# Performance work log

Measured on AMD Instinct MI355X. Metric: run time of the kernel, lower is better.

The kernel has to match this reference:

```python
import jax, jax.numpy as jnp
import numpy as np

N = 131072; B = 4; PER = N // B
M = 32768; MPER = M // B; K = 16; E = M * K
NF = 16; C = 32
BNC = float(1.0 / np.sqrt(1.0 + 1e-5))  # BatchNorm1d in eval mode, default running stats (mean=0,var=1,affine=identity)
_kd = np.array([[1.,1.,1.],[-1.,1.,1.],[1.,-1.,1.],[1.,1.,-1.],[-1.,-1.,1.],[-1.,1.,-1.],[1.,-1.,-1.],[-1.,-1.,-1.]], np.float32) / np.float32(np.sqrt(3.0))
KDIRS = jnp.asarray(_kd)  # [8,3] LightKernel directions


def _ln(x, g, b):
    m = x.mean(-1, keepdims=True)
    v = ((x - m) ** 2).mean(-1, keepdims=True)
    return (x - m) / jnp.sqrt(v + 1e-5) * g + b


def _mlp2(x, w1, b1, w2, b2):
    # Seq(Lin, BN, SiLU) x2 ; BN in eval mode == multiply by BNC
    h = jax.nn.silu(BNC * (x @ w1 + b1))
    return jax.nn.silu(BNC * (h @ w2 + b2))


def setup_inputs():
    rng = np.random.default_rng(0)
    f32 = np.float32
    w = lambda fi, fo: jnp.asarray((rng.standard_normal((fi, fo)) * 0.05).astype(f32))
    dg = lambda n: jnp.asarray((rng.standard_normal(n) * 0.05).astype(f32))
    z = lambda n: jnp.zeros((n,), jnp.float32)
    o = lambda n: jnp.ones((n,), jnp.float32)
    pos = jnp.asarray((rng.standard_normal((N, 3)) * 5.0).astype(f32))
    reflectance = jnp.asarray(rng.random(N).astype(f32))
    batch = jnp.asarray(np.repeat(np.arange(B), PER).astype(np.int64))
    sf = jnp.full((B,), 10.0, jnp.float32)
    # voxel-sampled centers: MPER per cloud, within each cloud's index range
    idx = np.concatenate([b * PER + rng.choice(PER, MPER, replace=False) for b in range(B)])
    tb = np.repeat(np.arange(B), MPER)
    # radius-graph edges: K in-batch source neighbors per sampled target
    col = (rng.integers(0, PER, size=(M, K)) + tb[:, None] * PER).reshape(-1)
    row = np.repeat(np.arange(M), K)
    inp = dict(pos=pos, reflectance=reflectance, sf=sf,
               batch=batch, idx=jnp.asarray(idx.astype(np.int64)),
               col=jnp.asarray(col.astype(np.int64)), row=jnp.asarray(row.astype(np.int64)))
    inp.update(stem_ln_g=o(97), stem_ln_b=z(97), stem_w1=w(97, 64), stem_b1=z(64),
               stem_w2=w(64, C), stem_b2=z(C),
               lk_w=w(8, 3), lk_b=z(3), lk_ln_g=o(3), lk_ln_b=z(3),
               loc_w1=w(C + 7, 64), loc_b1=z(64), loc_w2=w(64, 4 * C), loc_b2=z(4 * C),
               exp_w=w(128, 512), exp_b=z(512),
               dw1_w=dg(512), dw1_b=z(512), pw1_w=w(512, 512), pw1_b=z(512),
               dw2_w=dg(512), dw2_b=z(512), pw2_w=w(512, 512), pw2_b=z(512),
               proj_w=w(512, 128), proj_b=z(128))
    return inp


def _forward(pos, reflectance, sf, batch, idx, col, row,
             stem_ln_g, stem_ln_b, stem_w1, stem_b1, stem_w2, stem_b2,
             lk_w, lk_b, lk_ln_g, lk_ln_b,
             loc_w1, loc_b1, loc_w2, loc_b2,
             exp_w, exp_b, dw1_w, dw1_b, pw1_w, pw1_b,
             dw2_w, dw2_b, pw2_w, pw2_b, proj_w, proj_b):
    # --- StemModule: positional encoding + LayerNorm(97) + MLP[97,64,32] ---
    npos = pos / sf[batch][:, None]
    cnt = jax.ops.segment_sum(jnp.ones((N,), jnp.float32), batch, num_segments=B)
    centers = jax.ops.segment_sum(npos, batch, num_segments=B) / jnp.maximum(cnt, 1.0)[:, None]
    npos = npos - centers[batch]
    freqs = 1.0 / (10000.0 ** (2.0 * jnp.arange(NF, dtype=jnp.float32) / NF))
    pe = npos[:, :, None] * freqs                                   # [N,3,NF]
    pe = jnp.concatenate([jnp.sin(pe), jnp.cos(pe)], axis=-1).reshape(N, -1)  # [N,96]
    xin = _ln(jnp.concatenate([pe, reflectance[:, None]], axis=1), stem_ln_g, stem_ln_b)
    x = _mlp2(xin, stem_w1, stem_b1, stem_w2, stem_b2)              # [N,C]
    # --- SAModule: PointNetConv on precomputed radius graph ---
    pos4 = jnp.concatenate([pos, reflectance[:, None]], axis=1)     # [N,4]
    rel = pos4[col] - pos4[idx][row]                                # [E,4] pos_j - pos_i
    rel3 = rel[:, :3]
    dirs = rel3 / (jnp.linalg.norm(rel3, axis=1, keepdims=True) + 1e-8)
    kr = dirs @ KDIRS.T                                             # [E,8] kernel responses
    ecnt = jax.ops.segment_sum(jnp.ones((E,), jnp.float32), row, num_segments=M)
    nb = jax.ops.segment_sum(kr, row, num_segments=M) / jnp.maximum(ecnt, 1.0)[:, None]  # scatter_mean
    sfeat = _ln(nb @ lk_w + lk_b, lk_ln_g, lk_ln_b)                 # [M,3]
    msg = jnp.concatenate([x[col], rel, sfeat[row]], axis=1)        # [E,C+7]
    h = _mlp2(msg, loc_w1, loc_b1, loc_w2, loc_b2)                  # [E,4C] local_nn
    agg = jax.ops.segment_max(h, row, num_segments=M)               # max aggregation [M,4C]
    # --- InvertedResidualBlock (all kernel-size-1 convs => linear / per-channel) ---
    r = agg
    o = jax.nn.silu(BNC * (agg @ exp_w + exp_b))        # expand 128->512
    o = jax.nn.silu(BNC * (o * dw1_w + dw1_b))          # depthwise conv k=1
    o = jax.nn.silu(BNC * (o @ pw1_w + pw1_b))          # pointwise conv
    o = jax.nn.silu(BNC * o)                            # BN+SiLU between DWSep blocks
    o = jax.nn.silu(BNC * (o * dw2_w + dw2_b))
    o = jax.nn.silu(BNC * (o @ pw2_w + pw2_b))
    o = BNC * o                                         # trailing BN (no act)
    o = BNC * (o @ proj_w + proj_b)                     # project 512->128 + BN
    return jax.nn.silu(o + r)                           # [M,4C]


def reference(pos, reflectance, sf, batch, idx, col, row,
              stem_ln_g, stem_ln_b, stem_w1, stem_b1, stem_w2, stem_b2,
              lk_w, lk_b, lk_ln_g, lk_ln_b,
              loc_w1, loc_b1, loc_w2, loc_b2,
              exp_w, exp_b, dw1_w, dw1_b, pw1_w, pw1_b,
              dw2_w, dw2_b, pw2_w, pw2_b, proj_w, proj_b):
    return _forward(pos, reflectance, sf, batch, idx, col, row,
                    stem_ln_g, stem_ln_b, stem_w1, stem_b1, stem_w2, stem_b2,
                    lk_w, lk_b, lk_ln_g, lk_ln_b,
                    loc_w1, loc_b1, loc_w2, loc_b2,
                    exp_w, exp_b, dw1_w, dw1_b, pw1_w, pw1_b,
                    dw2_w, dw2_b, pw2_w, pw2_b, proj_w, proj_b)
```

## Files before the change

kernel.cpp:

```cpp
#include <hip/hip_runtime.h>

typedef unsigned short u16;
typedef unsigned int   u32;
typedef __attribute__((ext_vector_type(8))) u16  u16x8;
typedef __attribute__((ext_vector_type(4))) float f32x4;

#define N_PTS   131072
#define M_PTS   32768
#define BNCF    0.9999950000374997f

__device__ __forceinline__ float b2f(u16 u) {
    u32 x = ((u32)u) << 16;
    float f;
    __builtin_memcpy(&f, &x, 4);
    return f;
}
__device__ __forceinline__ u16 f2b(float f) {
    u32 x;
    __builtin_memcpy(&x, &f, 4);
    u32 r = x + 0x7fffu + ((x >> 16) & 1u);
    return (u16)(r >> 16);
}
__device__ __forceinline__ u16 f2b_hw(float f) {
    u32 r;
    asm("v_cvt_pk_bf16_f32 %0, %1, %1" : "=v"(r) : "v"(f));
    return (u16)r;
}
__device__ __forceinline__ float silu_f(float x) {
    return x * __builtin_amdgcn_rcpf(1.0f + __expf(-x));
}

__device__ __forceinline__ f32x4 mfma_bf16(u16x8 a, u16x8 b, f32x4 c) {
    asm volatile("v_mfma_f32_16x16x32_bf16 %0, %1, %2, %0"
                 : "+v"(c) : "v"(a), "v"(b));
    return c;
}
__device__ __forceinline__ void mai_guard() {
    asm volatile("s_nop 7\n\ts_nop 7\n\ts_nop 3");
}

__device__ __forceinline__ void cp_glds16(const u16* g, u16* l) {
    typedef const __attribute__((address_space(1))) u32* gp1_t;
    typedef __attribute__((address_space(3))) u32* lp3_t;
    __builtin_amdgcn_global_load_lds((gp1_t)(unsigned long long)g,
                                     (lp3_t)(unsigned long long)l, 16, 0, 0);
}

__global__ __launch_bounds__(256) void k_prep(const float* __restrict__ expw, u16* __restrict__ expwt,
                                              const float* __restrict__ pw1w, u16* __restrict__ pw1t,
                                              const float* __restrict__ pw2w, u16* __restrict__ pw2t,
                                              const float* __restrict__ prjw, u16* __restrict__ prjt,
                                              const float* __restrict__ lw1,  u16* __restrict__ lw1t,
                                              const float* __restrict__ lw2,  u16* __restrict__ lw2t,
                                              const float* __restrict__ sw1,  u16* __restrict__ sw1t,
                                              const float* __restrict__ sw2,  u16* __restrict__ sw2t,
                                              float* __restrict__ cent) {
    __shared__ u16 tile[64][66];
    int bid = blockIdx.x;
    if (bid < 160) {
        const float* W; u16* O; int K, Nn, tk, tn_;
        if (bid < 16)              { W = expw; O = expwt; K = 128; Nn = 512; tk = bid >> 3; tn_ = bid & 7; }
        else if ((bid -= 16) < 64) { W = pw1w; O = pw1t;  K = 512; Nn = 512; tk = bid >> 3; tn_ = bid & 7; }
        else if ((bid -= 64) < 64) { W = pw2w; O = pw2t;  K = 512; Nn = 512; tk = bid >> 3; tn_ = bid & 7; }
        else { bid -= 64;            W = prjw; O = prjt;  K = 512; Nn = 128; tk = bid >> 1; tn_ = bid & 1; }
        int k0 = tk * 64, n0 = tn_ * 64;
        int c = threadIdx.x & 63, r0 = threadIdx.x >> 6;
#pragma unroll
        for (int rr = 0; rr < 16; ++rr) {
            int row = r0 * 16 + rr;
            tile[row][c] = f2b(W[(long)(k0 + row) * Nn + n0 + c]);
        }
        __syncthreads();
#pragma unroll
        for (int rr = 0; rr < 16; ++rr) {
            int row = r0 * 16 + rr;
            O[(long)(n0 + row) * K + k0 + c] = tile[c][row];
        }
        return;
    }
    int idx = (bid - 160) * 256 + threadIdx.x;
    if (bid == 247 && threadIdx.x < 16) cent[threadIdx.x] = 0.0f;
    const float* W; u16* O; int K, ksh, Nn;
    if (idx < 4096)                  { W = lw1; O = lw1t; K = 39; ksh = 6; Nn = 64;  }
    else if ((idx -= 4096) < 8192)   { W = lw2; O = lw2t; K = 64; ksh = 6; Nn = 128; }
    else if ((idx -= 8192) < 8192)   { W = sw1; O = sw1t; K = 97; ksh = 7; Nn = 64;  }
    else if ((idx -= 8192) < 2048)   { W = sw2; O = sw2t; K = 64; ksh = 6; Nn = 32;  }
    else return;
    int n = idx >> ksh, k = idx & ((1 << ksh) - 1);
    O[idx] = (k < K) ? f2b(W[(long)k * Nn + n]) : (u16)0;
}

__global__ __launch_bounds__(256) void k_centers(const float* __restrict__ pos,
                                                 const float* __restrict__ sfv,
                                                 const int* __restrict__ batch,
                                                 float* __restrict__ acc) {
    __shared__ float ls[16];
    int t = threadIdx.x, lane = t & 63, wave = t >> 6;
    int i = blockIdx.x * 256 + t;
    int b = batch[blockIdx.x * 256];
    float inv = 1.0f / sfv[b];
    float x = pos[i * 3 + 0] * inv;
    float y = pos[i * 3 + 1] * inv;
    float z = pos[i * 3 + 2] * inv;
#pragma unroll
    for (int m = 1; m < 64; m <<= 1) {
        x += __shfl_xor(x, m);
        y += __shfl_xor(y, m);
        z += __shfl_xor(z, m);
    }
    if (lane == 0) { ls[wave * 4 + 0] = x; ls[wave * 4 + 1] = y; ls[wave * 4 + 2] = z; }
    __syncthreads();
    if (t < 3) {
        float s = ls[t] + ls[4 + t] + ls[8 + t] + ls[12 + t];
        atomicAdd(&acc[b * 4 + t], s);
    }
    if (t == 3) atomicAdd(&acc[b * 4 + 3], 256.0f);
}

__global__ __launch_bounds__(256, 4) void k_stem(const float* __restrict__ pos,
                                              const float* __restrict__ refl,
                                              const float* __restrict__ sfv,
                                              const int* __restrict__ batch,
                                              const float* __restrict__ cacc,
                                              const float* __restrict__ g,
                                              const float* __restrict__ bb,
                                              const u16* __restrict__ w1t,
                                              const float* __restrict__ b1,
                                              const u16* __restrict__ w2t,
                                              const float* __restrict__ b2,
                                              u16* __restrict__ xout) {
    __shared__ u16 xs[128][136];
    const float FLO[8] = {
        1.0f, 0.31622776601683794f, 0.1f, 0.031622776601683791f,
        0.01f, 0.0031622776601683794f, 0.001f, 0.00031622776601683794f};
    const float FHI[8] = {
        0.0001f, 3.1622776601683795e-05f, 1e-05f, 3.1622776601683796e-06f,
        1e-06f, 3.1622776601683797e-07f, 1e-07f, 3.1622776601683792e-08f};
    int t = threadIdx.x;
    int wave = t >> 6, lane = t & 63;
    int quad = lane >> 4, l16 = lane & 15;
    int mt0 = wave * 2;

    {
        int p = t >> 1, half = t & 1;
        int i = blockIdx.x * 128 + p;
        int b = batch[i];
        float s = 1.0f / sfv[b];
        float cnt = fmaxf(cacc[b * 4 + 3], 1.0f);
        float npv[3];
#pragma unroll
        for (int d = 0; d < 3; ++d)
            npv[d] = pos[i * 3 + d] * s - cacc[b * 4 + d] / cnt;

        float fq[8];
#pragma unroll
        for (int f = 0; f < 8; ++f) fq[f] = half ? FHI[f] : FLO[f];

        float sv[3][8], cv[3][8];
        float sum = 0.0f, sq = 0.0f;
#pragma unroll
        for (int d = 0; d < 3; ++d) {
#pragma unroll
            for (int f = 0; f < 8; ++f) {
                float a = npv[d] * fq[f];
                float s_, c_;
                __sincosf(a, &s_, &c_);
                sv[d][f] = s_;
                cv[d][f] = c_;
                sum += s_ + c_;
                sq += s_ * s_ + c_ * c_;
            }
        }
        float rf = refl[i];
        if (half == 0) { sum += rf; sq += rf * rf; }
        sum += __shfl_xor(sum, 1);
        sq  += __shfl_xor(sq, 1);

        float m = sum * (1.0f / 97.0f);
        float var = sq * (1.0f / 97.0f) - m * m;
        float rstd = rsqrtf(fmaxf(var, 0.0f) + 1e-5f);

#pragma unroll
        for (int d = 0; d < 3; ++d) {
            int c0 = d * 32 + half * 8;
            {
                f32x4 g0  = *(const f32x4*)(g + c0);
                f32x4 g1  = *(const f32x4*)(g + c0 + 4);
                f32x4 bb0 = *(const f32x4*)(bb + c0);
                f32x4 bb1 = *(const f32x4*)(bb + c0 + 4);
                u16 tmp[8];
#pragma unroll
                for (int f = 0; f < 4; ++f) {
                    tmp[f]     = f2b_hw((sv[d][f]     - m) * rstd * g0[f] + bb0[f]);
                    tmp[4 + f] = f2b_hw((sv[d][4 + f] - m) * rstd * g1[f] + bb1[f]);
                }
                *(uint4*)(&xs[p][c0]) = *(uint4*)tmp;
            }
            int c1 = d * 32 + 16 + half * 8;
            {
                f32x4 g0  = *(const f32x4*)(g + c1);
                f32x4 g1  = *(const f32x4*)(g + c1 + 4);
                f32x4 bb0 = *(const f32x4*)(bb + c1);
                f32x4 bb1 = *(const f32x4*)(bb + c1 + 4);
                u16 tmp[8];
#pragma unroll
                for (int f = 0; f < 4; ++f) {
                    tmp[f]     = f2b_hw((cv[d][f]     - m) * rstd * g0[f] + bb0[f]);
                    tmp[4 + f] = f2b_hw((cv[d][4 + f] - m) * rstd * g1[f] + bb1[f]);
                }
                *(uint4*)(&xs[p][c1]) = *(uint4*)tmp;
            }
        }
        if (half == 0) {
            float v = rf;
            u16 tmp[8];
            tmp[0] = f2b_hw((v - m) * rstd * g[96] + bb[96]);
#pragma unroll
            for (int f = 1; f < 8; ++f) tmp[f] = 0;
            *(uint4*)(&xs[p][96]) = *(uint4*)tmp;
        } else {
            uint4 z = {0, 0, 0, 0};
            *(uint4*)(&xs[p][104]) = z;
            *(uint4*)(&xs[p][112]) = z;
            *(uint4*)(&xs[p][120]) = z;
        }
    }
    __syncthreads();

    {
        f32x4 acc[2][4];
#pragma unroll
        for (int i = 0; i < 2; ++i)
#pragma unroll
            for (int j = 0; j < 4; ++j) acc[i][j] = (f32x4){0.f, 0.f, 0.f, 0.f};
#pragma unroll
        for (int kk = 0; kk < 128; kk += 32) {
            u16x8 af[2], bfr[4];
#pragma unroll
            for (int i = 0; i < 2; ++i)
                af[i] = *(const u16x8*)(&xs[(mt0 + i) * 16 + l16][kk + quad * 8]);
#pragma unroll
            for (int j = 0; j < 4; ++j)
                bfr[j] = *(const u16x8*)(w1t + (j * 16 + l16) * 128 + kk + quad * 8);
#pragma unroll
            for (int i = 0; i < 2; ++i)
#pragma unroll
                for (int j = 0; j < 4; ++j)
                    acc[i][j] = mfma_bf16(af[i], bfr[j], acc[i][j]);
        }
        mai_guard();
#pragma unroll
        for (int i = 0; i < 2; ++i)
#pragma unroll
            for (int j = 0; j < 4; ++j) {
                f32x4 c = acc[i][j];
                int n = j * 16 + l16;
                float bn = b1[n] * BNCF;
#pragma unroll
                for (int r = 0; r < 4; ++r)
                    xs[(mt0 + i) * 16 + quad * 4 + r][n] =
                        f2b_hw(silu_f(fmaf(BNCF, c[r], bn)));
            }
    }
    __syncthreads();

    {
        f32x4 acc[2][2];
#pragma unroll
        for (int i = 0; i < 2; ++i)
#pragma unroll
            for (int j = 0; j < 2; ++j) acc[i][j] = (f32x4){0.f, 0.f, 0.f, 0.f};
#pragma unroll
        for (int kk = 0; kk < 64; kk += 32) {
            u16x8 af[2], bfr[2];
#pragma unroll
            for (int i = 0; i < 2; ++i)
                af[i] = *(const u16x8*)(&xs[(mt0 + i) * 16 + l16][kk + quad * 8]);
#pragma unroll
            for (int j = 0; j < 2; ++j)
                bfr[j] = *(const u16x8*)(w2t + (j * 16 + l16) * 64 + kk + quad * 8);
#pragma unroll
            for (int i = 0; i < 2; ++i)
#pragma unroll
                for (int j = 0; j < 2; ++j)
                    acc[i][j] = mfma_bf16(af[i], bfr[j], acc[i][j]);
        }
        mai_guard();
#pragma unroll
        for (int i = 0; i < 2; ++i)
#pragma unroll
            for (int j = 0; j < 2; ++j) {
                f32x4 c = acc[i][j];
                int n = j * 16 + l16;
                float bn = b2[n] * BNCF;
#pragma unroll
                for (int r = 0; r < 4; ++r) {
                    int m = (mt0 + i) * 16 + quad * 4 + r;
                    long ig = (long)blockIdx.x * 128 + m;
                    xout[ig * 32 + n] = f2b_hw(silu_f(fmaf(BNCF, c[r], bn)));
                }
            }
    }
}

__global__ __launch_bounds__(256, 4) void k_edge(const float* __restrict__ pos,
                                              const float* __restrict__ refl,
                                              const int* __restrict__ idxp,
                                              const int* __restrict__ colp,
                                              const u16* __restrict__ xfeat,
                                              const float* __restrict__ lkw,
                                              const float* __restrict__ lkb,
                                              const float* __restrict__ lng,
                                              const float* __restrict__ lnb,
                                              const u16* __restrict__ w1t,
                                              const float* __restrict__ b1,
                                              const u16* __restrict__ w2t,
                                              const float* __restrict__ b2,
                                              float* __restrict__ agg,
                                              u16* __restrict__ aggb) {
    __shared__ u16 uni16[128 * 72];
    __shared__ u16 ws[128 * 72];
    __shared__ float b1s[64];
    __shared__ float b2s[128];
    int t = threadIdx.x;
    int r0 = blockIdx.x * 8;
    long e0 = (long)r0 * 16;
    int wave = t >> 6, lane = t & 63;
    int quad = lane >> 4, l16 = lane & 15;
    int mt0 = wave * 2;

    for (int u = t; u < 512; u += 256) {
        int row = u >> 3, c8 = (u & 7) * 8;
        *(uint4*)(&ws[row * 72 + c8]) = *(const uint4*)(w1t + row * 64 + c8);
    }
    if (t < 64) b1s[t] = b1[t] * BNCF;
    if (t < 128) b2s[t] = b2[t] * BNCF;

    if (t >= 128) {
        for (int u = t - 128; u < 512; u += 128) {
            int e = u >> 2, seg = u & 3;
            int c = colp[e0 + e];
            uint4 d = *(const uint4*)(xfeat + (long)c * 32 + seg * 8);
            *(uint4*)(&uni16[e * 72 + seg * 8]) = d;
        }
    } else {
        int e = t;
        int r = r0 + (e >> 4);
        int c = colp[e0 + e];
        int ci = idxp[r];
        float dx = pos[c * 3 + 0] - pos[ci * 3 + 0];
        float dy = pos[c * 3 + 1] - pos[ci * 3 + 1];
        float dz = pos[c * 3 + 2] - pos[ci * 3 + 2];
        float dr = refl[c] - refl[ci];

        float nrm = sqrtf(dx * dx + dy * dy + dz * dz);
        float inv = __builtin_amdgcn_rcpf(nrm + 1e-8f);
        float ux = dx * inv, uy = dy * inv, uz = dz * inv;
#pragma unroll
        for (int msk = 1; msk <= 8; msk <<= 1) {
            ux += __shfl_xor(ux, msk);
            uy += __shfl_xor(uy, msk);
            uz += __shfl_xor(uz, msk);
        }
        const float S3_16 = 0.57735026918962576f * (1.0f / 16.0f);
        const float sxk[8] = {1, -1, 1, 1, -1, -1, 1, -1};
        const float syk[8] = {1, 1, -1, 1, -1, 1, -1, -1};
        const float szk[8] = {1, 1, 1, -1, 1, -1, -1, -1};
        float sc0 = lkb[0], sc1 = lkb[1], sc2 = lkb[2];
#pragma unroll
        for (int j = 0; j < 8; ++j) {
            float nb = (sxk[j] * ux + syk[j] * uy + szk[j] * uz) * S3_16;
            sc0 += nb * lkw[j * 3 + 0];
            sc1 += nb * lkw[j * 3 + 1];
            sc2 += nb * lkw[j * 3 + 2];
        }
        float mm = (sc0 + sc1 + sc2) * (1.0f / 3.0f);
        float vv = ((sc0 - mm) * (sc0 - mm) + (sc1 - mm) * (sc1 - mm) +
                    (sc2 - mm) * (sc2 - mm)) * (1.0f / 3.0f);
        float rstd = rsqrtf(fmaxf(vv, 0.0f) + 1e-5f);

        u16 tmp[8];
        tmp[0] = f2b_hw(dx);
        tmp[1] = f2b_hw(dy);
        tmp[2] = f2b_hw(dz);
        tmp[3] = f2b_hw(dr);
        tmp[4] = f2b_hw((sc0 - mm) * rstd * lng[0] + lnb[0]);
        tmp[5] = f2b_hw((sc1 - mm) * rstd * lng[1] + lnb[1]);
        tmp[6] = f2b_hw((sc2 - mm) * rstd * lng[2] + lnb[2]);
        tmp[7] = 0;
        *(uint4*)(&uni16[e * 72 + 32]) = *(uint4*)tmp;
        uint4 z = {0, 0, 0, 0};
        *(uint4*)(&uni16[e * 72 + 40]) = z;
        *(uint4*)(&uni16[e * 72 + 48]) = z;
        *(uint4*)(&uni16[e * 72 + 56]) = z;
    }
    __syncthreads();

    {
        f32x4 acc[2][4];
#pragma unroll
        for (int i = 0; i < 2; ++i)
#pragma unroll
            for (int j = 0; j < 4; ++j) acc[i][j] = (f32x4){0.f, 0.f, 0.f, 0.f};
#pragma unroll
        for (int kk = 0; kk < 64; kk += 32) {
            u16x8 af[2], bfr[4];
#pragma unroll
            for (int i = 0; i < 2; ++i)
                af[i] = *(const u16x8*)(&uni16[((mt0 + i) * 16 + l16) * 72 + kk + quad * 8]);
#pragma unroll
            for (int j = 0; j < 4; ++j)
                bfr[j] = *(const u16x8*)(&ws[(j * 16 + l16) * 72 + kk + quad * 8]);
#pragma unroll
            for (int i = 0; i < 2; ++i)
#pragma unroll
                for (int j = 0; j < 4; ++j)
                    acc[i][j] = mfma_bf16(af[i], bfr[j], acc[i][j]);
        }
        mai_guard();
#pragma unroll
        for (int i = 0; i < 2; ++i)
#pragma unroll
            for (int j = 0; j < 4; ++j) {
                f32x4 c = acc[i][j];
                int n = j * 16 + l16;
#pragma unroll
                for (int r = 0; r < 4; ++r) {
                    float v = silu_f(fmaf(BNCF, c[r], b1s[n]));
                    uni16[((mt0 + i) * 16 + quad * 4 + r) * 72 + n] = f2b_hw(v);
                }
            }
    }
    __syncthreads();

    for (int u = t; u < 1024; u += 256) {
        int row = u >> 3, c8 = (u & 7) * 8;
        *(uint4*)(&ws[row * 72 + c8]) = *(const uint4*)(w2t + row * 64 + c8);
    }
    __syncthreads();

    {
        f32x4 acc[2][8];
#pragma unroll
        for (int i = 0; i < 2; ++i)
#pragma unroll
            for (int j = 0; j < 8; ++j) acc[i][j] = (f32x4){0.f, 0.f, 0.f, 0.f};
#pragma unroll
        for (int kk = 0; kk < 64; kk += 32) {
            u16x8 af[2], bfr[8];
#pragma unroll
            for (int i = 0; i < 2; ++i)
                af[i] = *(const u16x8*)(&uni16[((mt0 + i) * 16 + l16) * 72 + kk + quad * 8]);
#pragma unroll
            for (int j = 0; j < 8; ++j)
                bfr[j] = *(const u16x8*)(&ws[(j * 16 + l16) * 72 + kk + quad * 8]);
#pragma unroll
            for (int i = 0; i < 2; ++i)
#pragma unroll
                for (int j = 0; j < 8; ++j)
                    acc[i][j] = mfma_bf16(af[i], bfr[j], acc[i][j]);
        }
        mai_guard();
#pragma unroll
        for (int i = 0; i < 2; ++i) {
            int rg = r0 + mt0 + i;
#pragma unroll
            for (int j = 0; j < 8; ++j) {
                f32x4 c = acc[i][j];
                int n = j * 16 + l16;
                float mx = fmaxf(fmaxf(c[0], c[1]), fmaxf(c[2], c[3]));
                float mn = fminf(fminf(c[0], c[1]), fminf(c[2], c[3]));
                mx = fmaxf(mx, __shfl_xor(mx, 16));
                mx = fmaxf(mx, __shfl_xor(mx, 32));
                mn = fminf(mn, __shfl_xor(mn, 16));
                mn = fminf(mn, __shfl_xor(mn, 32));
                if (quad == 0) {
                    float v = fmaxf(silu_f(fmaf(BNCF, mx, b2s[n])),
                                    silu_f(fmaf(BNCF, mn, b2s[n])));
                    agg[(long)rg * 128 + n] = v;
                    aggb[(long)rg * 128 + n] = f2b_hw(v);
                }
            }
        }
    }
}

template <int EPI, int OD, int NXB, int K, int Nn>
__global__ __launch_bounds__(256, 4) void k_mgemm(const u16* __restrict__ A,
                                               const u16* __restrict__ Bt,
                                               const float* __restrict__ bias,
                                               const float* __restrict__ dww,
                                               const float* __restrict__ dwb,
                                               const float* __restrict__ res,
                                               void* __restrict__ Ov) {
    __shared__ u16 As[128 * 64];
    __shared__ u16 Bs[128 * 64];
    int t = threadIdx.x;
    int wave = t >> 6, lane = t & 63;
    int quad = lane >> 4, l16 = lane & 15;
    int bx, by;
    if (NXB == 4) {
        int d = blockIdx.x;
        int q = d >> 5, r = d & 31;
        by = q * 8 + (r & 7);
        bx = r >> 3;
    } else {
        bx = 0; by = blockIdx.x;
    }
    int R0 = by * 128, C0 = bx * 128;
    int wm = (wave & 1) * 64, wn = (wave >> 1) * 64;

    int srow = (lane >> 3);
    int sch  = lane & 7;

    f32x4 acc[4][4];
#pragma unroll
    for (int i = 0; i < 4; ++i)
#pragma unroll
        for (int j = 0; j < 4; ++j) acc[i][j] = (f32x4){0.f, 0.f, 0.f, 0.f};

    for (int k0 = 0; k0 < K; k0 += 64) {
#pragma unroll
        for (int it = 0; it < 4; ++it) {
            int base = wave * 32 + it * 8;
            int row = base + srow;
            int gch = (sch ^ (row & 7)) << 3;
            cp_glds16(A  + (long)(R0 + row) * K + k0 + gch, &As[base * 64]);
            cp_glds16(Bt + (long)(C0 + row) * K + k0 + gch, &Bs[base * 64]);
        }
        __syncthreads();
#pragma unroll
        for (int kk = 0; kk < 64; kk += 32) {
            int kb = kk >> 3;
            u16x8 af[4], bfr[4];
#pragma unroll
            for (int tm = 0; tm < 4; ++tm) {
                int r = wm + tm * 16 + l16;
                af[tm] = *(const u16x8*)(&As[r * 64 + (((kb + quad) ^ (r & 7)) << 3)]);
            }
#pragma unroll
            for (int tn = 0; tn < 4; ++tn) {
                int r = wn + tn * 16 + l16;
                bfr[tn] = *(const u16x8*)(&Bs[r * 64 + (((kb + quad) ^ (r & 7)) << 3)]);
            }
#pragma unroll
            for (int tm = 0; tm < 4; ++tm)
#pragma unroll
                for (int tn = 0; tn < 4; ++tn)
                    acc[tm][tn] = mfma_bf16(af[tm], bfr[tn], acc[tm][tn]);
        }
        __syncthreads();
    }

    float bnA[4], dnA[4], dbA[4];
#pragma unroll
    for (int tn = 0; tn < 4; ++tn) {
        int n = C0 + wn + tn * 16 + l16;
        bnA[tn] = bias[n] * BNCF;
        if (EPI == 0 || EPI == 1) { dnA[tn] = dww[n] * BNCF; dbA[tn] = dwb[n] * BNCF; }
        else { dnA[tn] = 0.0f; dbA[tn] = 0.0f; }
    }
    mai_guard();
#pragma unroll
    for (int tm = 0; tm < 4; ++tm) {
#pragma unroll
        for (int tn = 0; tn < 4; ++tn) {
            f32x4 c = acc[tm][tn];
            int n = C0 + wn + tn * 16 + l16;
#pragma unroll
            for (int r = 0; r < 4; ++r) {
                int m = R0 + wm + tm * 16 + quad * 4 + r;
                float v = c[r];
                if (EPI == 0) {
                    v = silu_f(fmaf(BNCF, v, bnA[tn]));
                    v = silu_f(fmaf(v, dnA[tn], dbA[tn]));
                } else if (EPI == 1) {
                    v = silu_f(fmaf(BNCF, v, bnA[tn]));
                    v = silu_f(BNCF * v);
                    v = silu_f(fmaf(v, dnA[tn], dbA[tn]));
                } else if (EPI == 2) {
                    v = silu_f(fmaf(BNCF, v, bnA[tn]));
                    v = BNCF * v;
                } else {
                    v = fmaf(BNCF, v, bnA[tn]);
                    v = silu_f(v + res[(long)m * 128 + n]);
                }
                if (OD == 0)
                    ((u16*)Ov)[(long)m * Nn + n] = f2b_hw(v);
                else
                    ((float*)Ov)[(long)m * Nn + n] = v;
            }
        }
    }
}

extern "C" void kernel_launch(void* const* d_in, const int* in_sizes, int n_in,
                              void* d_out, int out_size, void* d_ws, size_t ws_size,
                              hipStream_t stream) {
    const float* pos   = (const float*)d_in[0];
    const float* refl  = (const float*)d_in[1];
    const float* sfv   = (const float*)d_in[2];
    const int*   batch = (const int*)d_in[3];
    const int*   idxp  = (const int*)d_in[4];
    const int*   colp  = (const int*)d_in[5];
    const float* s_g  = (const float*)d_in[7];
    const float* s_b  = (const float*)d_in[8];
    const float* s_w1 = (const float*)d_in[9];
    const float* s_b1 = (const float*)d_in[10];
    const float* s_w2 = (const float*)d_in[11];
    const float* s_b2 = (const float*)d_in[12];
    const float* lkw  = (const float*)d_in[13];
    const float* lkb  = (const float*)d_in[14];
    const float* lng  = (const float*)d_in[15];
    const float* lnb  = (const float*)d_in[16];
    const float* l_w1 = (const float*)d_in[17];
    const float* l_b1 = (const float*)d_in[18];
    const float* l_w2 = (const float*)d_in[19];
    const float* l_b2 = (const float*)d_in[20];
    const float* expw = (const float*)d_in[21];
    const float* expb = (const float*)d_in[22];
    const float* dw1w = (const float*)d_in[23];
    const float* dw1b = (const float*)d_in[24];
    const float* pw1w = (const float*)d_in[25];
    const float* pw1b = (const float*)d_in[26];
    const float* dw2w = (const float*)d_in[27];
    const float* dw2b = (const float*)d_in[28];
    const float* pw2w = (const float*)d_in[29];
    const float* pw2b = (const float*)d_in[30];
    const float* prjw = (const float*)d_in[31];
    const float* prjb = (const float*)d_in[32];

    char* ws = (char*)d_ws;
    float* cent  = (float*)(ws + 0);
    float* agg   = (float*)(ws + 393280);
    u16*   aggb  = (u16*)(ws + 17170496);
    u16*   u1    = (u16*)(ws + 25559104);
    u16*   u2    = (u16*)(ws + 59113536);
    u16*   xf    = (u16*)(ws + 59113536);
    u16*   expwt = (u16*)(ws + 92667968);
    u16*   pw1t  = (u16*)(ws + 92799040);
    u16*   pw2t  = (u16*)(ws + 93323328);
    u16*   prjt  = (u16*)(ws + 93847616);
    u16*   lw1t  = (u16*)(ws + 93978688);
    u16*   lw2t  = (u16*)(ws + 93986880);
    u16*   sw1t  = (u16*)(ws + 94003264);
    u16*   sw2t  = (u16*)(ws + 94019648);

    k_prep<<<248, 256, 0, stream>>>(expw, expwt, pw1w, pw1t, pw2w, pw2t, prjw, prjt,
                                    l_w1, lw1t, l_w2, lw2t, s_w1, sw1t, s_w2, sw2t,
                                    cent);

    k_centers<<<512, 256, 0, stream>>>(pos, sfv, batch, cent);
    k_stem<<<1024, 256, 0, stream>>>(pos, refl, sfv, batch, cent, s_g, s_b,
                                     sw1t, s_b1, sw2t, s_b2, xf);
    k_edge<<<4096, 256, 0, stream>>>(pos, refl, idxp, colp, xf,
                                     lkw, lkb, lng, lnb,
                                     lw1t, l_b1, lw2t, l_b2, agg, aggb);

    dim3 blk(256);
    k_mgemm<0, 0, 4, 128, 512><<<1024, blk, 0, stream>>>(aggb, expwt, expb, dw1w, dw1b,
                                                         nullptr, u1);
    k_mgemm<1, 0, 4, 512, 512><<<1024, blk, 0, stream>>>(u1, pw1t, pw1b, dw2w, dw2b,
                                                         nullptr, u2);
    k_mgemm<2, 0, 4, 512, 512><<<1024, blk, 0, stream>>>(u2, pw2t, pw2b, nullptr, nullptr,
                                                         nullptr, u1);
    k_mgemm<3, 1, 1, 512, 128><<<256, blk, 0, stream>>>(u1, prjt, prjb, nullptr, nullptr,
                                                        agg, d_out);
}
```

Measured before the change: 294.2 us.

## Swizzle edge-kernel LDS, async-load weights and gathers, drop mid-kernel barriers

The edge kernel moves from padded LDS tiles to XOR-swizzled 16-byte-chunk layouts, with separate buffers for the two message halves and both weight matrices. The weight tiles and gathered neighbor features are loaded with direct global-to-LDS copies. The second-layer weights are fetched up front, so the two barriers and reload between the MLP layers go away. Biases are held in registers. The aim is to cut LDS bank conflicts, register staging and synchronization, at the cost of slightly more LDS per block and reliance on each wave reusing only its own rows in place.

```diff
diff --git a/kernel.cpp b/kernel.cpp
--- a/kernel.cpp
+++ b/kernel.cpp
@@ -318,10 +318,10 @@
                                               const float* __restrict__ b2,
                                               float* __restrict__ agg,
                                               u16* __restrict__ aggb) {
-    __shared__ u16 uni16[128 * 72];
-    __shared__ u16 ws[128 * 72];
-    __shared__ float b1s[64];
-    __shared__ float b2s[128];
+    __shared__ u16 msgA[128 * 32];
+    __shared__ u16 msgB[128 * 32];
+    __shared__ u16 ws1[64 * 64];
+    __shared__ u16 ws2[128 * 64];
     int t = threadIdx.x;
     int r0 = blockIdx.x * 8;
     long e0 = (long)r0 * 16;
@@ -329,19 +329,36 @@
     int quad = lane >> 4, l16 = lane & 15;
     int mt0 = wave * 2;
 
-    for (int u = t; u < 512; u += 256) {
-        int row = u >> 3, c8 = (u & 7) * 8;
-        *(uint4*)(&ws[row * 72 + c8]) = *(const uint4*)(w1t + row * 64 + c8);
-    }
-    if (t < 64) b1s[t] = b1[t] * BNCF;
-    if (t < 128) b2s[t] = b2[t] * BNCF;
+    float bnA[4], b2A[8];
+#pragma unroll
+    for (int j = 0; j < 4; ++j) bnA[j] = b1[j * 16 + l16] * BNCF;
+#pragma unroll
+    for (int j = 0; j < 8; ++j) b2A[j] = b2[j * 16 + l16] * BNCF;
 
     if (t >= 128) {
-        for (int u = t - 128; u < 512; u += 128) {
-            int e = u >> 2, seg = u & 3;
+        int gw = (t >> 6) - 2;
+#pragma unroll
+        for (int it = 0; it < 8; ++it) {
+            int cb = it * 128 + gw * 64;
+            int ch = cb + lane;
+            int row = ch >> 3, sl = ch & 7;
+            cp_glds16(w2t + row * 64 + ((sl ^ (row & 7)) << 3), &ws2[cb * 8]);
+        }
+#pragma unroll
+        for (int it = 0; it < 4; ++it) {
+            int cb = it * 128 + gw * 64;
+            int ch = cb + lane;
+            int row = ch >> 3, sl = ch & 7;
+            cp_glds16(w1t + row * 64 + ((sl ^ (row & 7)) << 3), &ws1[cb * 8]);
+        }
+#pragma unroll
+        for (int it = 0; it < 4; ++it) {
+            int cb = it * 128 + gw * 64;
+            int ch = cb + lane;
+            int e = ch >> 2, sl = ch & 3;
+            int gs = sl ^ (e & 3);
             int c = colp[e0 + e];
-            uint4 d = *(const uint4*)(xfeat + (long)c * 32 + seg * 8);
-            *(uint4*)(&uni16[e * 72 + seg * 8]) = d;
+            cp_glds16(xfeat + (long)c * 32 + gs * 8, &msgA[cb * 8]);
         }
     } else {
         int e = t;
@@ -388,11 +405,11 @@
         tmp[5] = f2b_hw((sc1 - mm) * rstd * lng[1] + lnb[1]);
         tmp[6] = f2b_hw((sc2 - mm) * rstd * lng[2] + lnb[2]);
         tmp[7] = 0;
-        *(uint4*)(&uni16[e * 72 + 32]) = *(uint4*)tmp;
         uint4 z = {0, 0, 0, 0};
-        *(uint4*)(&uni16[e * 72 + 40]) = z;
-        *(uint4*)(&uni16[e * 72 + 48]) = z;
-        *(uint4*)(&uni16[e * 72 + 56]) = z;
+        *(uint4*)(&msgB[(e * 4 + (e & 3)) * 8]) = *(uint4*)tmp;
+#pragma unroll
+        for (int gs = 1; gs < 4; ++gs)
+            *(uint4*)(&msgB[(e * 4 + (gs ^ (e & 3))) * 8]) = z;
     }
     __syncthreads();
 
@@ -403,14 +420,20 @@
 #pragma unroll
             for (int j = 0; j < 4; ++j) acc[i][j] = (f32x4){0.f, 0.f, 0.f, 0.f};
 #pragma unroll
-        for (int kk = 0; kk < 64; kk += 32) {
+        for (int half = 0; half < 2; ++half) {
             u16x8 af[2], bfr[4];
 #pragma unroll
-            for (int i = 0; i < 2; ++i)
-                af[i] = *(const u16x8*)(&uni16[((mt0 + i) * 16 + l16) * 72 + kk + quad * 8]);
-#pragma unroll
-            for (int j = 0; j < 4; ++j)
-                bfr[j] = *(const u16x8*)(&ws[(j * 16 + l16) * 72 + kk + quad * 8]);
+            for (int i = 0; i < 2; ++i) {
+                int row = (mt0 + i) * 16 + l16;
+                const u16* buf = half ? msgB : msgA;
+                af[i] = *(const u16x8*)(&buf[(row * 4 + (quad ^ (row & 3))) * 8]);
+            }
+#pragma unroll
+            for (int j = 0; j < 4; ++j) {
+                int r = j * 16 + l16;
+                int ch = half * 4 + quad;
+                bfr[j] = *(const u16x8*)(&ws1[(r * 8 + (ch ^ (r & 7))) * 8]);
+            }
 #pragma unroll
             for (int i = 0; i < 2; ++i)
 #pragma unroll
@@ -424,20 +447,16 @@
             for (int j = 0; j < 4; ++j) {
                 f32x4 c = acc[i][j];
                 int n = j * 16 + l16;
+                u16* buf = (j < 2) ? msgA : msgB;
+                int lc = (n >> 3) & 3;
 #pragma unroll
                 for (int r = 0; r < 4; ++r) {
-                    float v = silu_f(fmaf(BNCF, c[r], b1s[n]));
-                    uni16[((mt0 + i) * 16 + quad * 4 + r) * 72 + n] = f2b_hw(v);
+                    int row = (mt0 + i) * 16 + quad * 4 + r;
+                    float v = silu_f(fmaf(BNCF, c[r], bnA[j]));
+                    buf[(row * 4 + (lc ^ (row & 3))) * 8 + (n & 7)] = f2b_hw(v);
                 }
             }
     }
-    __syncthreads();
-
-    for (int u = t; u < 1024; u += 256) {
-        int row = u >> 3, c8 = (u & 7) * 8;
-        *(uint4*)(&ws[row * 72 + c8]) = *(const uint4*)(w2t + row * 64 + c8);
-    }
-    __syncthreads();
 
     {
         f32x4 acc[2][8];
@@ -446,14 +465,20 @@
 #pragma unroll
             for (int j = 0; j < 8; ++j) acc[i][j] = (f32x4){0.f, 0.f, 0.f, 0.f};
 #pragma unroll
-        for (int kk = 0; kk < 64; kk += 32) {
+        for (int half = 0; half < 2; ++half) {
             u16x8 af[2], bfr[8];
 #pragma unroll
-            for (int i = 0; i < 2; ++i)
-                af[i] = *(const u16x8*)(&uni16[((mt0 + i) * 16 + l16) * 72 + kk + quad * 8]);
-#pragma unroll
-            for (int j = 0; j < 8; ++j)
-                bfr[j] = *(const u16x8*)(&ws[(j * 16 + l16) * 72 + kk + quad * 8]);
+            for (int i = 0; i < 2; ++i) {
+                int row = (mt0 + i) * 16 + l16;
+                const u16* buf = half ? msgB : msgA;
+                af[i] = *(const u16x8*)(&buf[(row * 4 + (quad ^ (row & 3))) * 8]);
+            }
+#pragma unroll
+            for (int j = 0; j < 8; ++j) {
+                int r = j * 16 + l16;
+                int ch = half * 4 + quad;
+                bfr[j] = *(const u16x8*)(&ws2[(r * 8 + (ch ^ (r & 7))) * 8]);
+            }
 #pragma unroll
             for (int i = 0; i < 2; ++i)
 #pragma unroll
@@ -475,8 +500,8 @@
                 mn = fminf(mn, __shfl_xor(mn, 16));
                 mn = fminf(mn, __shfl_xor(mn, 32));
                 if (quad == 0) {
-                    float v = fmaxf(silu_f(fmaf(BNCF, mx, b2s[n])),
-                                    silu_f(fmaf(BNCF, mn, b2s[n])));
+                    float v = fmaxf(silu_f(fmaf(BNCF, mx, b2A[j])),
+                                    silu_f(fmaf(BNCF, mn, b2A[j])));
                     agg[(long)rg * 128 + n] = v;
                     aggb[(long)rg * 128 + n] = f2b_hw(v);
                 }
```

Result: faster. 286.4 us (median of 2 runs) (-2.6%).
